# Optimization experiments

Hardware: AMD Instinct MI355X
Metric: run time of the kernel (lower is better)

## Reference

```python
import jax, jax.numpy as jnp
import numpy as np

G, N, H, OUT, L = 16, 96, 128, 1, 3
DEG = 16
E = G * N * DEG


def setup_inputs() -> dict:
    key = jax.random.key(0)
    ks = iter(jax.random.split(key, 64))
    x = jax.random.randint(next(ks), (G * N, 9), 0, 2)
    edge_attr = jax.random.randint(next(ks), (E, 3), 0, 2)
    # edges grouped per graph (matches PyG batching); global node ids
    edge_graph = jnp.repeat(jnp.arange(G), E // G)
    edge_src = edge_graph * N + jax.random.randint(next(ks), (E,), 0, N)
    edge_dst = edge_graph * N + jax.random.randint(next(ks), (E,), 0, N)

    def lin(shape, fan_in):
        return jax.random.normal(next(ks), shape, jnp.float32) / np.sqrt(fan_in)

    return dict(
        x=x, edge_attr=edge_attr, edge_src=edge_src, edge_dst=edge_dst,
        num_graphs=G, max_nodes=N,
        atom_tables=jax.random.normal(next(ks), (9, 119, H)) * 0.02,
        bond_tables=jax.random.normal(next(ks), (3, 6, H)) * 0.02,
        W_m1=lin((L, 2, 2 * H, H), 2 * H), b_m1=jnp.zeros((L, 2, H)),
        W_m2=lin((L, 2, 2 * H, H), 2 * H), b_m2=jnp.zeros((L, 2, H)),
        W_me=lin((L, 2, H, H), H), b_me=jnp.zeros((L, 2, H)),
        W_mg=lin((L, 2, H, H), H), b_mg=jnp.zeros((L, 2, H)),
        W_mlp1=lin((L, 2, H, H), H), b_mlp1=jnp.zeros((L, 2, H)),
        W_mlp2=lin((L, 2, H, H), H), b_mlp2=jnp.zeros((L, 2, H)),
        W_o1=lin((L, 2, 2 * H, H), 2 * H), b_o1=jnp.zeros((L, 2, H)),
        W_o2=lin((L, 2, H, H), H), b_o2=jnp.zeros((L, 2, H)),
        ln_g=jnp.ones((L, 2, H)), ln_b=jnp.zeros((L, 2, H)),
        W_red=lin((L, 2 * H, H), 2 * H), b_red=jnp.zeros((L, H)),
        W_p1=lin((H, H), H), b_p1=jnp.zeros((H,)),
        W_p2=lin((H, OUT), H), b_p2=jnp.zeros((OUT,)),
    )


def _forward(x, edge_attr, edge_src, edge_dst, num_graphs, max_nodes,
             atom_tables, bond_tables, W_m1, b_m1, W_m2, b_m2, W_me, b_me,
             W_mg, b_mg, W_mlp1, b_mlp1, W_mlp2, b_mlp2, W_o1, b_o1,
             W_o2, b_o2, ln_g, ln_b, W_red, b_red, W_p1, b_p1, W_p2, b_p2):
    Hd = atom_tables.shape[-1]
    # OGB encoders: sum of per-column embeddings
    node_fts = atom_tables[jnp.arange(9)[:, None], x.T].sum(0)          # [G*N, H]
    edge_fts = bond_tables[jnp.arange(3)[:, None], edge_attr.T].sum(0)  # [E, H]
    node = node_fts.reshape(num_graphs, max_nodes, Hd)                  # to_dense_batch (equal-size graphs)
    # per-graph localization of global edge ids (== subtracting per-graph min)
    g = edge_src // max_nodes
    li = edge_src % max_nodes
    lj = edge_dst % max_nodes
    edge_dense = jnp.zeros((num_graphs, max_nodes, max_nodes, Hd),
                           node.dtype).at[g, li, lj].set(edge_fts)      # [G,N,N,H]
    graph_fts = jnp.zeros((num_graphs, Hd), node.dtype)
    hidden = jnp.zeros_like(node)
    for i in range(W_m1.shape[0]):
        outs = []
        for s in range(2):  # random / pretrained streams
            z = jnp.concatenate([node, hidden], -1)                     # [G,N,2H]
            msg1 = z @ W_m1[i, s] + b_m1[i, s]                          # [G,N,H]
            msg2 = z @ W_m2[i, s] + b_m2[i, s]
            msge = edge_dense @ W_me[i, s] + b_me[i, s]                 # [G,N,N,H]
            msgg = graph_fts @ W_mg[i, s] + b_mg[i, s]                  # [G,H]
            msgs = (msg1[:, None, :, :] + msg2[:, :, None, :]
                    + msge + msgg[:, None, None, :])
            m = jax.nn.relu(msgs)
            m = jax.nn.relu(m @ W_mlp1[i, s] + b_mlp1[i, s])
            msgs = m @ W_mlp2[i, s] + b_mlp2[i, s]
            # adj_mat is all ones -> masked max reduces to plain max over senders
            msgs = msgs.max(axis=1)                                     # [G,N,H]
            ret = z @ W_o1[i, s] + b_o1[i, s] + msgs @ W_o2[i, s] + b_o2[i, s]
            ret = jax.nn.relu(ret)
            mu = ret.mean(-1, keepdims=True)
            var = jnp.mean((ret - mu) ** 2, -1, keepdims=True)
            ret = (ret - mu) / jnp.sqrt(var + 1e-5) * ln_g[i, s] + ln_b[i, s]
            outs.append(ret)
        hidden = jnp.concatenate(outs, -1) @ W_red[i] + b_red[i]
    emb = hidden.mean(1)                                                # [G,H]
    h = jax.nn.relu(emb @ W_p1 + b_p1)
    return h @ W_p2 + b_p2                                              # [G,OUT]


def reference(x, edge_attr, edge_src, edge_dst, num_graphs, max_nodes,
              atom_tables, bond_tables, W_m1, b_m1, W_m2, b_m2, W_me, b_me,
              W_mg, b_mg, W_mlp1, b_mlp1, W_mlp2, b_mlp2, W_o1, b_o1,
              W_o2, b_o2, ln_g, ln_b, W_red, b_red, W_p1, b_p1, W_p2, b_p2):
    return _forward(x, edge_attr, edge_src, edge_dst, num_graphs, max_nodes,
                    atom_tables, bond_tables, W_m1, b_m1, W_m2, b_m2, W_me, b_me,
                    W_mg, b_mg, W_mlp1, b_mlp1, W_mlp2, b_mlp2, W_o1, b_o1,
                    W_o2, b_o2, ln_g, ln_b, W_red, b_red, W_p1, b_p1, W_p2, b_p2)
```

## Files before the change

kernel.cpp:

```cpp
#include <hip/hip_runtime.h>
#include <cstddef>

typedef _Float16 f16;
typedef f16 f16x8 __attribute__((ext_vector_type(8)));
typedef f16 f16x4 __attribute__((ext_vector_type(4)));
typedef float f32x4 __attribute__((ext_vector_type(4)));

constexpr int NG    = 16;
constexpr int NNODE = 96;
constexpr int TOTN  = 1536;
constexpr int HD    = 128;
constexpr int NEDGE = 24576;
constexpr int NLAY  = 3;

__device__ __forceinline__ f32x4 mfma16(f16x8 a, f16x8 b, f32x4 c) {
    return __builtin_amdgcn_mfma_f32_16x16x32_f16(a, b, c, 0, 0, 0);
}

__global__ void k_embed_nodes(const int* x, const float* atab, f16* zA) {
    const int v = blockIdx.x, h = threadIdx.x;
    float s = 0.f;
    for (int c = 0; c < 9; ++c)
        s += atab[((size_t)(c * 119 + x[v * 9 + c])) * HD + h];
    const size_t base = ((size_t)(v >> 4) * 32);
    zA[((base + (h >> 3)) * 16 + (v & 15)) * 8 + (h & 7)] = (f16)s;
    zA[((base + 16 + (h >> 3)) * 16 + (v & 15)) * 8 + (h & 7)] = (f16)0.f;
}

__global__ void k_embed_edges(const int* ea, const float* btab, f16* eftsA) {
    const int e = blockIdx.x, h = threadIdx.x;
    float s = 0.f;
    for (int c = 0; c < 3; ++c)
        s += btab[((size_t)(c * 6 + ea[e * 3 + c])) * HD + h];
    eftsA[(((size_t)(e >> 4) * 16 + (h >> 3)) * 16 + (e & 15)) * 8 + (h & 7)] = (f16)s;
}

__global__ void k_winit(int* winner) {
    winner[blockIdx.x * 256 + threadIdx.x] = -1;
}

__global__ void k_winner(const int* esrc, const int* edst, int* winner) {
    const int e = blockIdx.x * 256 + threadIdx.x;
    const int sg = esrc[e];
    const int g = sg / NNODE;
    const int li = sg - g * NNODE;
    const int lj = edst[e] - g * NNODE;
    atomicMax(&winner[((size_t)g * NNODE + li) * NNODE + lj], e);
}

__global__ void k_wswz(const float* Wm1, const float* Wm2, const float* Wo1,
                       const float* Wred, const float* Wo2, const float* W1,
                       const float* W2, const float* We,
                       f16* sm1, f16* sm2, f16* so1, f16* sred, f16* so2,
                       f16* s1, f16* s2, f16* sme) {
    const int idx = blockIdx.x * 256 + threadIdx.x;
    const int S256 = 6 * 256 * 128;
    const int SRED = 3 * 256 * 128;
    const int S128 = 6 * 128 * 128;
    const float* src;
    f16* dst;
    int rel, sh;
    if (idx < S256)                   { src = Wm1;  dst = sm1;  rel = idx;              sh = 15; }
    else if (idx < 2 * S256)          { src = Wm2;  dst = sm2;  rel = idx - S256;       sh = 15; }
    else if (idx < 3 * S256)          { src = Wo1;  dst = so1;  rel = idx - 2 * S256;   sh = 15; }
    else if (idx < 3 * S256 + SRED)   { src = Wred; dst = sred; rel = idx - 3 * S256;   sh = 15; }
    else if (idx < 3 * S256 + SRED + S128)
        { src = Wo2; dst = so2; rel = idx - 3 * S256 - SRED; sh = 14; }
    else if (idx < 3 * S256 + SRED + 2 * S128)
        { src = W1;  dst = s1;  rel = idx - 3 * S256 - SRED - S128; sh = 14; }
    else if (idx < 3 * S256 + SRED + 3 * S128)
        { src = W2;  dst = s2;  rel = idx - 3 * S256 - SRED - 2 * S128; sh = 14; }
    else if (idx < 3 * S256 + SRED + 4 * S128)
        { src = We;  dst = sme; rel = idx - 3 * S256 - SRED - 3 * S128; sh = 14; }
    else return;
    const int mat = rel >> sh;
    const int r2 = rel & ((1 << sh) - 1);
    const int k = r2 >> 7, n = r2 & 127;
    dst[(size_t)mat * (1 << sh) + (((k >> 3) * 128 + n) << 3) + (k & 7)] = (f16)src[rel];
}

__global__ __launch_bounds__(256) void k_ngemm(
    const f16* __restrict__ zA,
    const f16* __restrict__ sm1, const f16* __restrict__ sm2, const f16* __restrict__ so1,
    const float* __restrict__ bm1, const float* __restrict__ bm2,
    const float* __restrict__ bme, const float* __restrict__ bmg,
    const float* __restrict__ bo1,
    float* __restrict__ msg1, float* __restrict__ msg2, float* __restrict__ o1buf,
    int layer) {
    const int tid = threadIdx.x, lane = tid & 63, w = tid >> 6;
    const int mr = lane & 15, q = lane >> 4;
    const int t0 = blockIdx.x;
    const int wh = blockIdx.y >> 1, s = blockIdx.y & 1, ls = layer * 2 + s;
    const f16* B;
    float* out;
    float bias[8];
    if (wh == 0) {
        B = sm1 + (size_t)ls * 32768; out = msg1 + (size_t)s * TOTN * HD;
        for (int nt = 0; nt < 8; ++nt) {
            const int col = nt * 16 + mr;
            bias[nt] = bm1[ls * HD + col] + bme[ls * HD + col] + bmg[ls * HD + col];
        }
    } else if (wh == 1) {
        B = sm2 + (size_t)ls * 32768; out = msg2 + (size_t)s * TOTN * HD;
        for (int nt = 0; nt < 8; ++nt) bias[nt] = bm2[ls * HD + nt * 16 + mr];
    } else {
        B = so1 + (size_t)ls * 32768; out = o1buf + (size_t)s * TOTN * HD;
        for (int nt = 0; nt < 8; ++nt) bias[nt] = bo1[ls * HD + nt * 16 + mr];
    }
    const size_t tIdx = (size_t)t0 * 4 + w;
    f32x4 acc[8];
#pragma unroll
    for (int nt = 0; nt < 8; ++nt) acc[nt] = (f32x4){0.f, 0.f, 0.f, 0.f};
#pragma unroll
    for (int kt = 0; kt < 8; ++kt) {
        const int kq = kt * 4 + q;
        f16x8 a = *(const f16x8*)&zA[((tIdx * 32 + kq) * 16 + mr) * 8];
        const f16* bp = B + ((size_t)kq * HD) * 8;
#pragma unroll
        for (int nt = 0; nt < 8; ++nt) {
            f16x8 bv = *(const f16x8*)(bp + (nt * 16 + mr) * 8);
            acc[nt] = mfma16(a, bv, acc[nt]);
        }
    }
#pragma unroll
    for (int nt = 0; nt < 8; ++nt) {
        const int col = nt * 16 + mr;
#pragma unroll
        for (int r = 0; r < 4; ++r) {
            const int row = t0 * 64 + w * 16 + q * 4 + r;
            out[(size_t)row * HD + col] = acc[nt][r] + bias[nt];
        }
    }
}

__global__ __launch_bounds__(256) void k_egemm(
    const f16* __restrict__ eftsA, const f16* __restrict__ sme,
    f16* __restrict__ emsg) {
    const int tid = threadIdx.x, lane = tid & 63, w = tid >> 6;
    const int mr = lane & 15, q = lane >> 4;
    const int ls = blockIdx.y;
    const f16* B = sme + (size_t)ls * 16384;
    f32x4 acc[2][8];
#pragma unroll
    for (int mt = 0; mt < 2; ++mt)
#pragma unroll
        for (int nt = 0; nt < 8; ++nt) acc[mt][nt] = (f32x4){0.f, 0.f, 0.f, 0.f};
#pragma unroll
    for (int kt = 0; kt < 4; ++kt) {
        const int kq = kt * 4 + q;
        f16x8 a0 = *(const f16x8*)&eftsA[(((size_t)(blockIdx.x * 8 + 2 * w + 0) * 16 + kq) * 16 + mr) * 8];
        f16x8 a1 = *(const f16x8*)&eftsA[(((size_t)(blockIdx.x * 8 + 2 * w + 1) * 16 + kq) * 16 + mr) * 8];
        const f16* bp = B + ((size_t)kq * HD) * 8;
#pragma unroll
        for (int nt = 0; nt < 8; ++nt) {
            f16x8 bv = *(const f16x8*)(bp + (nt * 16 + mr) * 8);
            acc[0][nt] = mfma16(a0, bv, acc[0][nt]);
            acc[1][nt] = mfma16(a1, bv, acc[1][nt]);
        }
    }
#pragma unroll
    for (int mt = 0; mt < 2; ++mt) {
        const int ebase = blockIdx.x * 128 + (2 * w + mt) * 16 + q * 4;
#pragma unroll
        for (int nt = 0; nt < 8; ++nt) {
            const int col = nt * 16 + mr;
#pragma unroll
            for (int r = 0; r < 4; ++r)
                emsg[((size_t)ls * NEDGE + ebase + r) * HD + col] = (f16)acc[mt][nt][r];
        }
    }
}

__global__ __launch_bounds__(256) void k_pairs(
    const float* __restrict__ msg1, const float* __restrict__ msg2,
    const f16* __restrict__ emsg, const int* __restrict__ winner,
    const f16* __restrict__ w1s, const float* __restrict__ bmlp1,
    const f16* __restrict__ w2s, const float* __restrict__ bmlp2,
    float* __restrict__ maxpart, int layer) {
    __shared__ __align__(16) f16 M2s[24 * 128];
    __shared__ __align__(16) f16 Qb[128 * 128];
    const int tid = threadIdx.x, lane = tid & 63, w = tid >> 6;
    const int mr = lane & 15, q = lane >> 4;
    const int jt = blockIdx.x, b = blockIdx.y, zz = blockIdx.z;
    const int cp = zz >> 1, s = zz & 1, ls = layer * 2 + s;
    const int j0 = jt * 16, i0 = cp * 24;
    const f16* EM = emsg + (size_t)ls * NEDGE * HD;
    const f16* W1 = w1s + (size_t)ls * HD * HD;
    const f16* W2 = w2s + (size_t)ls * HD * HD;
    for (int idx = tid * 4; idx < 24 * 128; idx += 1024) {
        const int row = idx >> 7, col = idx & 127;
        float4 v = *(const float4*)&msg2[((size_t)s * TOTN + b * NNODE + i0 + row) * HD + col];
        f16x4 h;
        h[0] = (f16)v.x; h[1] = (f16)v.y; h[2] = (f16)v.z; h[3] = (f16)v.w;
        *(f16x4*)&M2s[idx] = h;
    }
    f16x8 m1f[4];
    {
        const float* m1p = msg1 + ((size_t)s * TOTN + b * NNODE + j0 + mr) * HD;
#pragma unroll
        for (int kt = 0; kt < 4; ++kt) {
            float4 p0 = *(const float4*)(m1p + kt * 32 + q * 8);
            float4 p1 = *(const float4*)(m1p + kt * 32 + q * 8 + 4);
            m1f[kt][0] = (f16)p0.x; m1f[kt][1] = (f16)p0.y;
            m1f[kt][2] = (f16)p0.z; m1f[kt][3] = (f16)p0.w;
            m1f[kt][4] = (f16)p1.x; m1f[kt][5] = (f16)p1.y;
            m1f[kt][6] = (f16)p1.z; m1f[kt][7] = (f16)p1.w;
        }
    }
    f16x8 Bf1[4][2], Bf2[4][2];
#pragma unroll
    for (int kt = 0; kt < 4; ++kt)
#pragma unroll
        for (int ntl = 0; ntl < 2; ++ntl) {
            const size_t off = ((size_t)(kt * 4 + q) * 128 + (2 * w + ntl) * 16 + mr) * 8;
            Bf1[kt][ntl] = *(const f16x8*)(W1 + off);
            Bf2[kt][ntl] = *(const f16x8*)(W2 + off);
        }
    float b1v[2], b2v[2];
#pragma unroll
    for (int ntl = 0; ntl < 2; ++ntl) {
        const int col = (2 * w + ntl) * 16 + mr;
        b1v[ntl] = bmlp1[ls * HD + col];
        b2v[ntl] = bmlp2[ls * HD + col];
    }
    float maxr[2][4];
#pragma unroll
    for (int ntl = 0; ntl < 2; ++ntl)
#pragma unroll
        for (int r = 0; r < 4; ++r) maxr[ntl][r] = -3.402823466e38f;
    __syncthreads();

    for (int it = 0; it < 3; ++it) {
        const int ibase = i0 + it * 8;
        int wv[8];
#pragma unroll
        for (int mt = 0; mt < 8; ++mt)
            wv[mt] = winner[((size_t)b * NNODE + ibase + mt) * NNODE + j0 + mr];
        f32x4 acc[8][2];
#pragma unroll
        for (int mt = 0; mt < 8; ++mt)
#pragma unroll
            for (int ntl = 0; ntl < 2; ++ntl) acc[mt][ntl] = (f32x4){0.f, 0.f, 0.f, 0.f};
#pragma unroll
        for (int kt = 0; kt < 4; ++kt) {
            const int ko = kt * 32 + q * 8;
#pragma unroll
            for (int mt = 0; mt < 8; ++mt) {
                f16x8 m2v = *(const f16x8*)&M2s[(it * 8 + mt) * 128 + ko];
                f16x8 av = m1f[kt] + m2v;
                if (wv[mt] >= 0) {
                    f16x8 ev = *(const f16x8*)&EM[(size_t)wv[mt] * HD + ko];
                    av = av + ev;
                }
#pragma unroll
                for (int u = 0; u < 8; ++u)
                    av[u] = av[u] > (f16)0.f ? av[u] : (f16)0.f;
                acc[mt][0] = mfma16(av, Bf1[kt][0], acc[mt][0]);
                acc[mt][1] = mfma16(av, Bf1[kt][1], acc[mt][1]);
            }
        }
#pragma unroll
        for (int mt = 0; mt < 8; ++mt)
#pragma unroll
            for (int ntl = 0; ntl < 2; ++ntl) {
                const int col = (2 * w + ntl) * 16 + mr;
                const int kg = col >> 3, kj = col & 7;
#pragma unroll
                for (int r = 0; r < 4; ++r) {
                    float v = fmaxf(acc[mt][ntl][r] + b1v[ntl], 0.f);
                    Qb[((mt * 16 + kg) * 16 + q * 4 + r) * 8 + kj] = (f16)v;
                }
            }
        __syncthreads();
#pragma unroll
        for (int mt = 0; mt < 8; ++mt)
#pragma unroll
            for (int ntl = 0; ntl < 2; ++ntl) acc[mt][ntl] = (f32x4){0.f, 0.f, 0.f, 0.f};
#pragma unroll
        for (int kt = 0; kt < 4; ++kt) {
#pragma unroll
            for (int mt = 0; mt < 8; ++mt) {
                f16x8 a = *(const f16x8*)&Qb[((mt * 16 + kt * 4 + q) * 16 + mr) * 8];
                acc[mt][0] = mfma16(a, Bf2[kt][0], acc[mt][0]);
                acc[mt][1] = mfma16(a, Bf2[kt][1], acc[mt][1]);
            }
        }
#pragma unroll
        for (int ntl = 0; ntl < 2; ++ntl)
#pragma unroll
            for (int r = 0; r < 4; ++r) {
                float m0 = acc[0][ntl][r];
#pragma unroll
                for (int mt = 1; mt < 8; ++mt) m0 = fmaxf(m0, acc[mt][ntl][r]);
                maxr[ntl][r] = fmaxf(maxr[ntl][r], m0 + b2v[ntl]);
            }
        __syncthreads();
    }
#pragma unroll
    for (int ntl = 0; ntl < 2; ++ntl) {
        const int col = (2 * w + ntl) * 16 + mr;
#pragma unroll
        for (int r = 0; r < 4; ++r) {
            const int j = j0 + q * 4 + r;
            maxpart[((size_t)zz * TOTN + b * NNODE + j) * HD + col] = maxr[ntl][r];
        }
    }
}

__global__ __launch_bounds__(256) void k_pr(
    const float* __restrict__ maxpart, const float* __restrict__ o1buf,
    const f16* __restrict__ so2, const float* __restrict__ bo2,
    const float* __restrict__ lng, const float* __restrict__ lnb,
    const f16* __restrict__ sred, const float* __restrict__ bred,
    float* __restrict__ hiddenf, f16* __restrict__ zA, int layer) {
    __shared__ __align__(16) f16 Af[16384];
    const int tid = threadIdx.x, lane = tid & 63, w = tid >> 6;
    const int mr = lane & 15, q = lane >> 4;
    const int row0 = blockIdx.x * 64;
    {
        const int mrow = tid >> 1, half = tid & 1;
        const int sb = mrow >> 6, rl = mrow & 63;
        const int row = row0 + rl;
#pragma unroll
        for (int c8 = 0; c8 < 64; c8 += 8) {
            const int col = half * 64 + c8;
            float mx[8] = {-3.4e38f, -3.4e38f, -3.4e38f, -3.4e38f,
                           -3.4e38f, -3.4e38f, -3.4e38f, -3.4e38f};
#pragma unroll
            for (int ch = 0; ch < 4; ++ch) {
                const float* p = maxpart + ((size_t)(ch * 2 + sb) * TOTN + row) * HD + col;
                float4 u0 = *(const float4*)p;
                float4 u1 = *(const float4*)(p + 4);
                mx[0] = fmaxf(mx[0], u0.x); mx[1] = fmaxf(mx[1], u0.y);
                mx[2] = fmaxf(mx[2], u0.z); mx[3] = fmaxf(mx[3], u0.w);
                mx[4] = fmaxf(mx[4], u1.x); mx[5] = fmaxf(mx[5], u1.y);
                mx[6] = fmaxf(mx[6], u1.z); mx[7] = fmaxf(mx[7], u1.w);
            }
            f16x8 pv;
#pragma unroll
            for (int u = 0; u < 8; ++u) pv[u] = (f16)mx[u];
            *(f16x8*)&Af[(((sb * 4 + (rl >> 4)) * 16 + (col >> 3)) * 16 + (rl & 15)) * 8] = pv;
        }
    }
    __syncthreads();
    const int sw = w >> 1, ls = layer * 2 + sw;
    const f16* B1 = so2 + (size_t)ls * 16384;
    f32x4 acc[2][8];
#pragma unroll
    for (int mt = 0; mt < 2; ++mt)
#pragma unroll
        for (int nt = 0; nt < 8; ++nt) acc[mt][nt] = (f32x4){0.f, 0.f, 0.f, 0.f};
#pragma unroll
    for (int kt = 0; kt < 4; ++kt) {
        const int kq = kt * 4 + q;
        f16x8 a0 = *(const f16x8*)&Af[(((sw * 4 + (w & 1) * 2 + 0) * 16 + kq) * 16 + mr) * 8];
        f16x8 a1 = *(const f16x8*)&Af[(((sw * 4 + (w & 1) * 2 + 1) * 16 + kq) * 16 + mr) * 8];
        const f16* bp = B1 + ((size_t)kq * HD) * 8;
#pragma unroll
        for (int nt = 0; nt < 8; ++nt) {
            f16x8 bv = *(const f16x8*)(bp + (nt * 16 + mr) * 8);
            acc[0][nt] = mfma16(a0, bv, acc[0][nt]);
            acc[1][nt] = mfma16(a1, bv, acc[1][nt]);
        }
    }
    float lngv[8], lnbv[8], bo2v[8];
#pragma unroll
    for (int nt = 0; nt < 8; ++nt) {
        const int col = nt * 16 + mr;
        lngv[nt] = lng[ls * HD + col];
        lnbv[nt] = lnb[ls * HD + col];
        bo2v[nt] = bo2[ls * HD + col];
    }
#pragma unroll
    for (int mt = 0; mt < 2; ++mt) {
#pragma unroll
        for (int nt = 0; nt < 8; ++nt) {
            const int col = nt * 16 + mr;
#pragma unroll
            for (int r = 0; r < 4; ++r) {
                const int rl = (w & 1) * 32 + mt * 16 + q * 4 + r;
                float v = acc[mt][nt][r] + bo2v[nt] +
                          o1buf[((size_t)sw * TOTN + row0 + rl) * HD + col];
                acc[mt][nt][r] = fmaxf(v, 0.f);
            }
        }
#pragma unroll
        for (int r = 0; r < 4; ++r) {
            float su = 0.f, sq = 0.f;
#pragma unroll
            for (int nt = 0; nt < 8; ++nt) {
                su += acc[mt][nt][r];
                sq += acc[mt][nt][r] * acc[mt][nt][r];
            }
#pragma unroll
            for (int mask = 1; mask <= 8; mask <<= 1) {
                su += __shfl_xor(su, mask, 64);
                sq += __shfl_xor(sq, mask, 64);
            }
            const float mean = su * (1.f / 128.f);
            float var = sq * (1.f / 128.f) - mean * mean;
            var = fmaxf(var, 0.f);
            const float rstd = 1.f / sqrtf(var + 1e-5f);
#pragma unroll
            for (int nt = 0; nt < 8; ++nt)
                acc[mt][nt][r] = (acc[mt][nt][r] - mean) * rstd * lngv[nt] + lnbv[nt];
        }
    }
    __syncthreads();
#pragma unroll
    for (int mt = 0; mt < 2; ++mt)
#pragma unroll
        for (int nt = 0; nt < 8; ++nt) {
            const int kg2 = sw * 16 + nt * 2 + (mr >> 3), j2 = mr & 7;
#pragma unroll
            for (int r = 0; r < 4; ++r) {
                const int rl = (w & 1) * 32 + mt * 16 + q * 4 + r;
                Af[(((rl >> 4) * 32 + kg2) * 16 + (rl & 15)) * 8 + j2] = (f16)acc[mt][nt][r];
            }
        }
    __syncthreads();
    const f16* B2 = sred + (size_t)layer * 32768;
    f32x4 a2[8];
#pragma unroll
    for (int nt = 0; nt < 8; ++nt) a2[nt] = (f32x4){0.f, 0.f, 0.f, 0.f};
#pragma unroll
    for (int kt = 0; kt < 8; ++kt) {
        const int kq = kt * 4 + q;
        f16x8 av = *(const f16x8*)&Af[((w * 32 + kq) * 16 + mr) * 8];
        const f16* bp = B2 + ((size_t)kq * HD) * 8;
#pragma unroll
        for (int nt = 0; nt < 8; ++nt) {
            f16x8 bv = *(const f16x8*)(bp + (nt * 16 + mr) * 8);
            a2[nt] = mfma16(av, bv, a2[nt]);
        }
    }
#pragma unroll
    for (int nt = 0; nt < 8; ++nt) {
        const int col = nt * 16 + mr;
        const float bb = bred[layer * HD + col];
#pragma unroll
        for (int r = 0; r < 4; ++r) {
            const int row = row0 + w * 16 + q * 4 + r;
            const float v = a2[nt][r] + bb;
            hiddenf[(size_t)row * HD + col] = v;
            zA[(((size_t)(row >> 4) * 32 + 16 + (col >> 3)) * 16 + (row & 15)) * 8 + (col & 7)] = (f16)v;
        }
    }
}

__global__ void k_final(const float* hiddenf, const float* Wp1, const float* bp1,
                        const float* Wp2, const float* bp2, float* out) {
    __shared__ float se[128];
    __shared__ float sr[128];
    const int b = blockIdx.x, h = threadIdx.x;
    float acc = 0.f;
    for (int v = 0; v < NNODE; ++v)
        acc += hiddenf[((size_t)b * NNODE + v) * HD + h];
    se[h] = acc * (1.f / 96.f);
    __syncthreads();
    float a2 = bp1[h];
    for (int k = 0; k < 128; ++k)
        a2 += se[k] * Wp1[(size_t)k * HD + h];
    a2 = fmaxf(a2, 0.f);
    sr[h] = a2 * Wp2[h];
    __syncthreads();
    for (int off = 64; off > 0; off >>= 1) {
        if (h < off) sr[h] += sr[h + off];
        __syncthreads();
    }
    if (h == 0) out[b] = sr[0] + bp2[0];
}

extern "C" void kernel_launch(void* const* d_in, const int* in_sizes, int n_in,
                              void* d_out, int out_size, void* d_ws, size_t ws_size,
                              hipStream_t stream) {
    (void)in_sizes; (void)n_in; (void)out_size; (void)ws_size;
    const int* x    = (const int*)d_in[0];
    const int* ea   = (const int*)d_in[1];
    const int* esrc = (const int*)d_in[2];
    const int* edst = (const int*)d_in[3];
    const float* atab = (const float*)d_in[6];
    const float* btab = (const float*)d_in[7];
    const float* Wm1 = (const float*)d_in[8];    const float* bm1 = (const float*)d_in[9];
    const float* Wm2 = (const float*)d_in[10];   const float* bm2 = (const float*)d_in[11];
    const float* Wme = (const float*)d_in[12];   const float* bme = (const float*)d_in[13];
    const float* bmg = (const float*)d_in[15];
    const float* Wmlp1 = (const float*)d_in[16]; const float* bmlp1 = (const float*)d_in[17];
    const float* Wmlp2 = (const float*)d_in[18]; const float* bmlp2 = (const float*)d_in[19];
    const float* Wo1 = (const float*)d_in[20];   const float* bo1 = (const float*)d_in[21];
    const float* Wo2 = (const float*)d_in[22];   const float* bo2 = (const float*)d_in[23];
    const float* lng = (const float*)d_in[24];   const float* lnb = (const float*)d_in[25];
    const float* Wred = (const float*)d_in[26];  const float* bred = (const float*)d_in[27];
    const float* Wp1 = (const float*)d_in[28];   const float* bp1 = (const float*)d_in[29];
    const float* Wp2 = (const float*)d_in[30];   const float* bp2 = (const float*)d_in[31];

    char* cur = (char*)d_ws;
    f16* zA = (f16*)cur;          cur += (size_t)TOTN * 256 * 2;
    float* hiddenf = (float*)cur; cur += (size_t)TOTN * HD * 4;
    f16* eftsA = (f16*)cur;       cur += (size_t)NEDGE * HD * 2;
    f16* emsg = (f16*)cur;        cur += (size_t)6 * NEDGE * HD * 2;
    float* msg1 = (float*)cur;    cur += (size_t)2 * TOTN * HD * 4;
    float* msg2 = (float*)cur;    cur += (size_t)2 * TOTN * HD * 4;
    float* o1buf = (float*)cur;   cur += (size_t)2 * TOTN * HD * 4;
    float* maxpart = (float*)cur; cur += (size_t)8 * TOTN * HD * 4;
    int* winner = (int*)cur;      cur += (size_t)NG * NNODE * NNODE * 4;
    f16* sw1 = (f16*)cur;         cur += (size_t)6 * HD * HD * 2;
    f16* sw2 = (f16*)cur;         cur += (size_t)6 * HD * HD * 2;
    f16* swme = (f16*)cur;        cur += (size_t)6 * HD * HD * 2;
    f16* swm1 = (f16*)cur;        cur += (size_t)6 * 256 * HD * 2;
    f16* swm2 = (f16*)cur;        cur += (size_t)6 * 256 * HD * 2;
    f16* swo1 = (f16*)cur;        cur += (size_t)6 * 256 * HD * 2;
    f16* swred = (f16*)cur;       cur += (size_t)3 * 256 * HD * 2;
    f16* swo2 = (f16*)cur;        cur += (size_t)6 * HD * HD * 2;

    k_winit<<<(NG * NNODE * NNODE) / 256, 256, 0, stream>>>(winner);
    k_embed_nodes<<<TOTN, 128, 0, stream>>>(x, atab, zA);
    k_embed_edges<<<NEDGE, 128, 0, stream>>>(ea, btab, eftsA);
    k_winner<<<NEDGE / 256, 256, 0, stream>>>(esrc, edst, winner);
    k_wswz<<<4224, 256, 0, stream>>>(Wm1, Wm2, Wo1, Wred, Wo2, Wmlp1, Wmlp2, Wme,
                                     swm1, swm2, swo1, swred, swo2, sw1, sw2, swme);
    k_egemm<<<dim3(192, 6), 256, 0, stream>>>(eftsA, swme, emsg);
    for (int layer = 0; layer < NLAY; ++layer) {
        k_ngemm<<<dim3(24, 6), 256, 0, stream>>>(zA, swm1, swm2, swo1,
                                                 bm1, bm2, bme, bmg, bo1,
                                                 msg1, msg2, o1buf, layer);
        k_pairs<<<dim3(6, NG, 8), 256, 0, stream>>>(msg1, msg2, emsg, winner,
                                                    sw1, bmlp1, sw2, bmlp2,
                                                    maxpart, layer);
        k_pr<<<24, 256, 0, stream>>>(maxpart, o1buf, swo2, bo2, lng, lnb,
                                     swred, bred, hiddenf, zA, layer);
    }
    k_final<<<NG, 128, 0, stream>>>(hiddenf, Wp1, bp1, Wp2, bp2, (float*)d_out);
}
```

Before: 472.4 us.

## Compact winning edge messages into per-block contiguous regions for pair kernel

Adds count/scan/assign kernels that give each winning edge a slot grouped by the (graph, j-tile, i-chunk) region of the k_pairs block that reads it. The edge GEMM writes only winning edges, scattered into that compacted layout, and k_pairs looks up messages through the new slot index. The aim is better locality for k_pairs' gathered edge-message loads and fewer emsg writes from the edge GEMM. The cost is three extra small kernels (including a single-thread serial scan over 384 regions) and a nondeterministic slot order within each region.

```diff
diff --git a/kernel.cpp b/kernel.cpp
--- a/kernel.cpp
+++ b/kernel.cpp
@@ -12,6 +12,7 @@
 constexpr int HD    = 128;
 constexpr int NEDGE = 24576;
 constexpr int NLAY  = 3;
+constexpr int NREG  = NG * 6 * 4;
 
 __device__ __forceinline__ f32x4 mfma16(f16x8 a, f16x8 b, f32x4 c) {
     return __builtin_amdgcn_mfma_f32_16x16x32_f16(a, b, c, 0, 0, 0);
@@ -35,8 +36,14 @@
     eftsA[(((size_t)(e >> 4) * 16 + (h >> 3)) * 16 + (e & 15)) * 8 + (h & 7)] = (f16)s;
 }
 
-__global__ void k_winit(int* winner) {
-    winner[blockIdx.x * 256 + threadIdx.x] = -1;
+__global__ void k_init(int* winner, int* winner2, int* eperm, int* cnt, int* base) {
+    const int idx = blockIdx.x * 256 + threadIdx.x;
+    if (idx < NG * NNODE * NNODE) {
+        winner[idx] = -1;
+        winner2[idx] = -1;
+    }
+    if (idx < NEDGE) eperm[idx] = -1;
+    if (idx < NREG) { cnt[idx] = 0; base[idx] = 0; }
 }
 
 __global__ void k_winner(const int* esrc, const int* edst, int* winner) {
@@ -46,6 +53,40 @@
     const int li = sg - g * NNODE;
     const int lj = edst[e] - g * NNODE;
     atomicMax(&winner[((size_t)g * NNODE + li) * NNODE + lj], e);
+}
+
+__device__ __forceinline__ int region_of(int idx) {
+    const int b = idx / (NNODE * NNODE);
+    const int r = idx - b * NNODE * NNODE;
+    const int i = r / NNODE, j = r - (r / NNODE) * NNODE;
+    return b * 24 + (j >> 4) * 4 + (i / 24);
+}
+
+__global__ void k_count(const int* winner, int* cnt) {
+    const int idx = blockIdx.x * 256 + threadIdx.x;
+    if (idx < NG * NNODE * NNODE && winner[idx] >= 0)
+        atomicAdd(&cnt[region_of(idx)], 1);
+}
+
+__global__ void k_scan(const int* cnt, int* base) {
+    if (threadIdx.x == 0) {
+        int s = 0;
+        for (int r = 0; r < NREG; ++r) {
+            base[r] = s;
+            s += cnt[r];
+        }
+    }
+}
+
+__global__ void k_assign(const int* winner, int* base, int* winner2, int* eperm) {
+    const int idx = blockIdx.x * 256 + threadIdx.x;
+    if (idx >= NG * NNODE * NNODE) return;
+    const int e = winner[idx];
+    if (e >= 0) {
+        const int p = atomicAdd(&base[region_of(idx)], 1);
+        winner2[idx] = p;
+        eperm[e] = p;
+    }
 }
 
 __global__ void k_wswz(const float* Wm1, const float* Wm2, const float* Wo1,
@@ -135,7 +176,7 @@
 
 __global__ __launch_bounds__(256) void k_egemm(
     const f16* __restrict__ eftsA, const f16* __restrict__ sme,
-    f16* __restrict__ emsg) {
+    const int* __restrict__ eperm, f16* __restrict__ emsgP) {
     const int tid = threadIdx.x, lane = tid & 63, w = tid >> 6;
     const int mr = lane & 15, q = lane >> 4;
     const int ls = blockIdx.y;
@@ -162,18 +203,20 @@
     for (int mt = 0; mt < 2; ++mt) {
         const int ebase = blockIdx.x * 128 + (2 * w + mt) * 16 + q * 4;
 #pragma unroll
-        for (int nt = 0; nt < 8; ++nt) {
-            const int col = nt * 16 + mr;
-#pragma unroll
-            for (int r = 0; r < 4; ++r)
-                emsg[((size_t)ls * NEDGE + ebase + r) * HD + col] = (f16)acc[mt][nt][r];
+        for (int r = 0; r < 4; ++r) {
+            const int p = eperm[ebase + r];
+            if (p < 0) continue;
+            f16* orow = emsgP + ((size_t)ls * NEDGE + p) * HD;
+#pragma unroll
+            for (int nt = 0; nt < 8; ++nt)
+                orow[nt * 16 + mr] = (f16)acc[mt][nt][r];
         }
     }
 }
 
 __global__ __launch_bounds__(256) void k_pairs(
     const float* __restrict__ msg1, const float* __restrict__ msg2,
-    const f16* __restrict__ emsg, const int* __restrict__ winner,
+    const f16* __restrict__ emsgP, const int* __restrict__ winner2,
     const f16* __restrict__ w1s, const float* __restrict__ bmlp1,
     const f16* __restrict__ w2s, const float* __restrict__ bmlp2,
     float* __restrict__ maxpart, int layer) {
@@ -184,7 +227,7 @@
     const int jt = blockIdx.x, b = blockIdx.y, zz = blockIdx.z;
     const int cp = zz >> 1, s = zz & 1, ls = layer * 2 + s;
     const int j0 = jt * 16, i0 = cp * 24;
-    const f16* EM = emsg + (size_t)ls * NEDGE * HD;
+    const f16* EM = emsgP + (size_t)ls * NEDGE * HD;
     const f16* W1 = w1s + (size_t)ls * HD * HD;
     const f16* W2 = w2s + (size_t)ls * HD * HD;
     for (int idx = tid * 4; idx < 24 * 128; idx += 1024) {
@@ -235,7 +278,7 @@
         int wv[8];
 #pragma unroll
         for (int mt = 0; mt < 8; ++mt)
-            wv[mt] = winner[((size_t)b * NNODE + ibase + mt) * NNODE + j0 + mr];
+            wv[mt] = winner2[((size_t)b * NNODE + ibase + mt) * NNODE + j0 + mr];
         f32x4 acc[8][2];
 #pragma unroll
         for (int mt = 0; mt < 8; ++mt)
@@ -498,12 +541,16 @@
     f16* zA = (f16*)cur;          cur += (size_t)TOTN * 256 * 2;
     float* hiddenf = (float*)cur; cur += (size_t)TOTN * HD * 4;
     f16* eftsA = (f16*)cur;       cur += (size_t)NEDGE * HD * 2;
-    f16* emsg = (f16*)cur;        cur += (size_t)6 * NEDGE * HD * 2;
+    f16* emsgP = (f16*)cur;       cur += (size_t)6 * NEDGE * HD * 2;
     float* msg1 = (float*)cur;    cur += (size_t)2 * TOTN * HD * 4;
     float* msg2 = (float*)cur;    cur += (size_t)2 * TOTN * HD * 4;
     float* o1buf = (float*)cur;   cur += (size_t)2 * TOTN * HD * 4;
     float* maxpart = (float*)cur; cur += (size_t)8 * TOTN * HD * 4;
     int* winner = (int*)cur;      cur += (size_t)NG * NNODE * NNODE * 4;
+    int* winner2 = (int*)cur;     cur += (size_t)NG * NNODE * NNODE * 4;
+    int* eperm = (int*)cur;       cur += (size_t)NEDGE * 4;
+    int* cnt = (int*)cur;         cur += (size_t)NREG * 4;
+    int* basep = (int*)cur;       cur += (size_t)NREG * 4;
     f16* sw1 = (f16*)cur;         cur += (size_t)6 * HD * HD * 2;
     f16* sw2 = (f16*)cur;         cur += (size_t)6 * HD * HD * 2;
     f16* swme = (f16*)cur;        cur += (size_t)6 * HD * HD * 2;
@@ -513,18 +560,22 @@
     f16* swred = (f16*)cur;       cur += (size_t)3 * 256 * HD * 2;
     f16* swo2 = (f16*)cur;        cur += (size_t)6 * HD * HD * 2;
 
-    k_winit<<<(NG * NNODE * NNODE) / 256, 256, 0, stream>>>(winner);
+    const int NPAIR = NG * NNODE * NNODE;
+    k_init<<<(NPAIR + 255) / 256, 256, 0, stream>>>(winner, winner2, eperm, cnt, basep);
     k_embed_nodes<<<TOTN, 128, 0, stream>>>(x, atab, zA);
     k_embed_edges<<<NEDGE, 128, 0, stream>>>(ea, btab, eftsA);
     k_winner<<<NEDGE / 256, 256, 0, stream>>>(esrc, edst, winner);
+    k_count<<<(NPAIR + 255) / 256, 256, 0, stream>>>(winner, cnt);
+    k_scan<<<1, 64, 0, stream>>>(cnt, basep);
+    k_assign<<<(NPAIR + 255) / 256, 256, 0, stream>>>(winner, basep, winner2, eperm);
     k_wswz<<<4224, 256, 0, stream>>>(Wm1, Wm2, Wo1, Wred, Wo2, Wmlp1, Wmlp2, Wme,
                                      swm1, swm2, swo1, swred, swo2, sw1, sw2, swme);
-    k_egemm<<<dim3(192, 6), 256, 0, stream>>>(eftsA, swme, emsg);
+    k_egemm<<<dim3(192, 6), 256, 0, stream>>>(eftsA, swme, eperm, emsgP);
     for (int layer = 0; layer < NLAY; ++layer) {
         k_ngemm<<<dim3(24, 6), 256, 0, stream>>>(zA, swm1, swm2, swo1,
                                                  bm1, bm2, bme, bmg, bo1,
                                                  msg1, msg2, o1buf, layer);
-        k_pairs<<<dim3(6, NG, 8), 256, 0, stream>>>(msg1, msg2, emsg, winner,
+        k_pairs<<<dim3(6, NG, 8), 256, 0, stream>>>(msg1, msg2, emsgP, winner2,
                                                     sw1, bmlp1, sw2, bmlp2,
                                                     maxpart, layer);
         k_pr<<<24, 256, 0, stream>>>(maxpart, o1buf, swo2, bo2, lng, lnb,
```

New measurement: 535.0 us. 13.2% more time.
